# Performance work log

Measured on AMD Instinct MI355X. Metric: run time of the kernel, lower is better.

Reference implementation:

```python
import jax, jax.numpy as jnp
import numpy as np
from jax import lax

B, T, D, LD, K = 128, 1024, 256, 512, 128
RD = LD + K  # 640 residual-LSTM width
PAD = 15     # (31 - 1) // 2 'same' padding for the LSA location conv


def _gru(x, h, wih, whh, bih, bhh):
    # torch.nn.GRUCell semantics, gate order [r, z, n]
    gi = x @ wih.T + bih
    gh = h @ whh.T + bhh
    ir, iz, inn = jnp.split(gi, 3, axis=-1)
    hr, hz, hn = jnp.split(gh, 3, axis=-1)
    r = jax.nn.sigmoid(ir + hr)
    z = jax.nn.sigmoid(iz + hz)
    n = jnp.tanh(inn + r * hn)
    return (1.0 - z) * n + z * h


def _lstm(x, h, c, wih, whh, bih, bhh):
    # torch.nn.LSTMCell semantics, gate order [i, f, g, o]
    g = x @ wih.T + bih + h @ whh.T + bhh
    i, f, gg, o = jnp.split(g, 4, axis=-1)
    c2 = jax.nn.sigmoid(f) * c + jax.nn.sigmoid(i) * jnp.tanh(gg)
    h2 = jax.nn.sigmoid(o) * jnp.tanh(c2)
    return h2, c2


def _forward(encoder_seq, encoder_seq_proj, prenet_in, attn_hidden, rnn1_h, rnn1_c,
             rnn2_h, rnn2_c, res_h, res_c, context_vec, cumulative, attn_prev,
             fc1_w, fc1_b, fc2_w, fc2_b, gru_wih, gru_whh, gru_bih, gru_bhh,
             conv_w, L_w, L_b, W_w, W_b, v_w, ri_w, ri_b,
             r1_wih, r1_whh, r1_bih, r1_bhh, r2_wih, r2_whh, r2_bih, r2_bhh,
             res_wih, res_whh, res_bih, res_bhh, stop_w, stop_b):
    # PreNet (dropout p = 0 in Decoder.__init__, so pure tanh-MLP)
    p = jnp.tanh(prenet_in @ fc1_w.T + fc1_b)
    prenet_out = jnp.tanh(p @ fc2_w.T + fc2_b)                     # [B, D//2]
    # Attention GRU
    attn_in = jnp.concatenate([context_vec, prenet_out], axis=-1)  # [B, D + D//2]
    attn_h = _gru(attn_in, attn_hidden, gru_wih, gru_whh, gru_bih, gru_bhh)  # [B, D]
    # LSA location-sensitive attention (cumulative/attn_prev are zeros at t=0)
    pq = (attn_h @ W_w.T + W_b)[:, None, :]                        # [B, 1, D]
    loc = jnp.stack([cumulative, attn_prev], axis=1)               # [B, 2, T]
    conv_out = lax.conv_general_dilated(loc, conv_w, (1,), [(PAD, PAD)],
                                        dimension_numbers=('NCH', 'OIH', 'NCH'))  # [B, 32, T]
    ploc = jnp.swapaxes(conv_out, 1, 2) @ L_w.T + L_b              # [B, T, D]
    u = jnp.squeeze(jnp.tanh(pq + encoder_seq_proj + ploc) @ v_w.T, -1)  # [B, T]
    sig = jax.nn.sigmoid(u)
    scores = sig / jnp.sum(sig, axis=1, keepdims=True)             # [B, T]
    cum_new = cumulative + scores
    context = jnp.einsum('bt,btd->bd', scores, encoder_seq)        # [B, D]
    # rnn_input projection + two residual LSTM cells (eval: no zoneout)
    x = jnp.concatenate([context, attn_h], axis=1) @ ri_w.T + ri_b  # [B, LD]
    h1, c1 = _lstm(x, rnn1_h, rnn1_c, r1_wih, r1_whh, r1_bih, r1_bhh)
    x = x + h1
    h2, c2 = _lstm(x, rnn2_h, rnn2_c, r2_wih, r2_whh, r2_bih, r2_bhh)
    x = x + h2
    # 4-layer residual LSTM stack on [prenet_in, x]
    res_x = jnp.concatenate([prenet_in, x], axis=1)                # [B, RD]
    hs, cs = [], []
    for i in range(4):
        hi, ci = _lstm(res_x, res_h[i], res_c[i], res_wih[i], res_whh[i], res_bih[i], res_bhh[i])
        res_x = res_x + hi
        hs.append(hi)
        cs.append(ci)
    cond = res_x                                                   # cond_features [B, RD]
    stop = jax.nn.sigmoid(cond @ stop_w.T + stop_b)                # [B, 1]
    return (cond, stop, scores, attn_h, h1, c1, h2, c2,
            jnp.stack(hs), jnp.stack(cs), context, cum_new)


def setup_inputs() -> dict:
    keys = iter(jax.random.split(jax.random.key(0), 64))
    nxt = lambda: next(keys)
    rn = lambda s: jax.random.normal(nxt(), s, jnp.float32)
    wp = lambda s: rn(s) * 0.02
    return {
        'encoder_seq': rn((B, T, D)),
        'encoder_seq_proj': rn((B, T, D)),
        'prenet_in': rn((B, K)),
        'attn_hidden': rn((B, D)),
        'rnn1_h': rn((B, LD)), 'rnn1_c': rn((B, LD)),
        'rnn2_h': rn((B, LD)), 'rnn2_c': rn((B, LD)),
        'res_h': rn((4, B, RD)), 'res_c': rn((4, B, RD)),
        'context_vec': rn((B, D)),
        'cumulative': jnp.zeros((B, T), jnp.float32),
        'attn_prev': jnp.zeros((B, T), jnp.float32),
        'fc1_w': wp((256, K)), 'fc1_b': jnp.zeros((256,), jnp.float32),
        'fc2_w': wp((D // 2, 256)), 'fc2_b': jnp.zeros((D // 2,), jnp.float32),
        'gru_wih': wp((3 * D, D + D // 2)), 'gru_whh': wp((3 * D, D)),
        'gru_bih': jnp.zeros((3 * D,), jnp.float32), 'gru_bhh': jnp.zeros((3 * D,), jnp.float32),
        'conv_w': wp((32, 2, 31)),
        'L_w': wp((D, 32)), 'L_b': jnp.zeros((D,), jnp.float32),
        'W_w': wp((D, D)), 'W_b': jnp.zeros((D,), jnp.float32),
        'v_w': wp((1, D)),
        'ri_w': wp((LD, 2 * D)), 'ri_b': jnp.zeros((LD,), jnp.float32),
        'r1_wih': wp((4 * LD, LD)), 'r1_whh': wp((4 * LD, LD)),
        'r1_bih': jnp.zeros((4 * LD,), jnp.float32), 'r1_bhh': jnp.zeros((4 * LD,), jnp.float32),
        'r2_wih': wp((4 * LD, LD)), 'r2_whh': wp((4 * LD, LD)),
        'r2_bih': jnp.zeros((4 * LD,), jnp.float32), 'r2_bhh': jnp.zeros((4 * LD,), jnp.float32),
        'res_wih': wp((4, 4 * RD, RD)), 'res_whh': wp((4, 4 * RD, RD)),
        'res_bih': jnp.zeros((4, 4 * RD), jnp.float32), 'res_bhh': jnp.zeros((4, 4 * RD), jnp.float32),
        'stop_w': wp((1, RD)), 'stop_b': jnp.zeros((1,), jnp.float32),
    }


def reference(encoder_seq, encoder_seq_proj, prenet_in, attn_hidden, rnn1_h, rnn1_c,
              rnn2_h, rnn2_c, res_h, res_c, context_vec, cumulative, attn_prev,
              fc1_w, fc1_b, fc2_w, fc2_b, gru_wih, gru_whh, gru_bih, gru_bhh,
              conv_w, L_w, L_b, W_w, W_b, v_w, ri_w, ri_b,
              r1_wih, r1_whh, r1_bih, r1_bhh, r2_wih, r2_whh, r2_bih, r2_bhh,
              res_wih, res_whh, res_bih, res_bhh, stop_w, stop_b):
    return _forward(encoder_seq, encoder_seq_proj, prenet_in, attn_hidden, rnn1_h, rnn1_c,
                    rnn2_h, rnn2_c, res_h, res_c, context_vec, cumulative, attn_prev,
                    fc1_w, fc1_b, fc2_w, fc2_b, gru_wih, gru_whh, gru_bih, gru_bhh,
                    conv_w, L_w, L_b, W_w, W_b, v_w, ri_w, ri_b,
                    r1_wih, r1_whh, r1_bih, r1_bhh, r2_wih, r2_whh, r2_bih, r2_bhh,
                    res_wih, res_whh, res_bih, res_bhh, stop_w, stop_b)
```

## Files before the change

### kernel.cpp

```cpp
#include <hip/hip_runtime.h>

#define DEV __device__ __forceinline__

typedef __attribute__((ext_vector_type(8))) short short8;
typedef __attribute__((ext_vector_type(4))) float f32x4;

DEV float fast_rcp(float x) { return __builtin_amdgcn_rcpf(x); }
DEV float sigm(float x) { return fast_rcp(1.0f + __expf(-x)); }
DEV float tanhf_fast(float x) { return 1.0f - 2.0f * fast_rcp(1.0f + __expf(2.0f * x)); }

DEV short f2bf(float f) {
    unsigned u = __float_as_uint(f);
    unsigned r = (u + 0x7FFFu + ((u >> 16) & 1u)) >> 16;
    return (short)r;
}

__global__ __launch_bounds__(256) void gemm2s_kernel(
    const float* __restrict__ A1, int K1, const float* __restrict__ W1, int ldw1,
    const float* __restrict__ A2, int K2, const float* __restrict__ W2, int ldw2,
    float* __restrict__ Cp, int N, int KS, int KC)
{
    __shared__ float As[2][16][128];
    __shared__ float Ws[2][16][33];
    const int tid = threadIdx.x;
    const int chunk = blockIdx.x % KS;
    const int n0 = (blockIdx.x / KS) * 32;
    const int kbeg = chunk * KC;
    const int nt = KC / 16;
    const int tx = tid & 15, ty = tid >> 4;
    const int lm = tid & 127, lk = (tid >> 7) * 8;

    float acc[16];
#pragma unroll
    for (int i = 0; i < 16; ++i) acc[i] = 0.f;

    float4 ra0, ra1, rw;
    auto load_regs = [&](int k0) {
        const float* A; const float* W; int lda, ldw, kc;
        if (k0 < K1) { A = A1; W = W1; lda = K1; ldw = ldw1; kc = k0; }
        else         { A = A2; W = W2; lda = K2; ldw = ldw2; kc = k0 - K1; }
        ra0 = *(const float4*)(A + (size_t)lm * lda + kc + lk);
        ra1 = *(const float4*)(A + (size_t)lm * lda + kc + lk + 4);
        if (tid < 128) {
            int nl = tid >> 2, kq = (tid & 3) * 4;
            rw = *(const float4*)(W + (size_t)(n0 + nl) * ldw + kc + kq);
        }
    };
    auto store_lds = [&](int buf) {
        As[buf][lk + 0][lm] = ra0.x; As[buf][lk + 1][lm] = ra0.y;
        As[buf][lk + 2][lm] = ra0.z; As[buf][lk + 3][lm] = ra0.w;
        As[buf][lk + 4][lm] = ra1.x; As[buf][lk + 5][lm] = ra1.y;
        As[buf][lk + 6][lm] = ra1.z; As[buf][lk + 7][lm] = ra1.w;
        if (tid < 128) {
            int nl = tid >> 2, kq = (tid & 3) * 4;
            Ws[buf][kq + 0][nl] = rw.x; Ws[buf][kq + 1][nl] = rw.y;
            Ws[buf][kq + 2][nl] = rw.z; Ws[buf][kq + 3][nl] = rw.w;
        }
    };

    load_regs(kbeg);
    store_lds(0);
    __syncthreads();

    for (int it = 0; it < nt; ++it) {
        const int cur = it & 1;
        if (it + 1 < nt) load_regs(kbeg + (it + 1) * 16);
#pragma unroll
        for (int kk = 0; kk < 16; ++kk) {
            float w0 = Ws[cur][kk][tx * 2 + 0];
            float w1 = Ws[cur][kk][tx * 2 + 1];
            float4 x0 = *(const float4*)&As[cur][kk][ty * 8];
            float4 x1 = *(const float4*)&As[cur][kk][ty * 8 + 4];
            acc[0] += x0.x * w0; acc[1] += x0.y * w0;
            acc[2] += x0.z * w0; acc[3] += x0.w * w0;
            acc[4] += x1.x * w0; acc[5] += x1.y * w0;
            acc[6] += x1.z * w0; acc[7] += x1.w * w0;
            acc[8]  += x0.x * w1; acc[9]  += x0.y * w1;
            acc[10] += x0.z * w1; acc[11] += x0.w * w1;
            acc[12] += x1.x * w1; acc[13] += x1.y * w1;
            acc[14] += x1.z * w1; acc[15] += x1.w * w1;
        }
        if (it + 1 < nt) store_lds(cur ^ 1);
        __syncthreads();
    }

    float* Co = Cp + (size_t)chunk * 128 * N;
#pragma unroll
    for (int j = 0; j < 2; ++j) {
        int n = n0 + tx * 2 + j;
#pragma unroll
        for (int i = 0; i < 8; ++i)
            Co[(size_t)(ty * 8 + i) * N + n] = acc[j * 8 + i];
    }
}

__global__ void reduce_act_kernel(const float* __restrict__ p, int KS, int MN,
                                  const float* __restrict__ b,
                                  float* __restrict__ out, int N, int act)
{
    int idx = blockIdx.x * 256 + threadIdx.x;
    if (idx >= MN) return;
    int n = idx % N;
    float v = b ? b[n] : 0.f;
    for (int s = 0; s < KS; ++s) v += p[(size_t)s * MN + idx];
    if (act) v = tanhf_fast(v);
    out[idx] = v;
}

__global__ void gru_gate_kernel(const float* __restrict__ gi_p, int KSi,
                                const float* __restrict__ gh_p, int KSh,
                                const float* __restrict__ bih, const float* __restrict__ bhh,
                                const float* __restrict__ h, float* __restrict__ out)
{
    const size_t MN = 128 * 768;
    int m = blockIdx.x, d = threadIdx.x;
    size_t base = (size_t)m * 768 + d;
    float ir = bih[d], iz = bih[256 + d], in = bih[512 + d];
    for (int s = 0; s < KSi; ++s) {
        const float* p = gi_p + s * MN + base;
        ir += p[0]; iz += p[256]; in += p[512];
    }
    float hr = bhh[d], hz = bhh[256 + d], hn = bhh[512 + d];
    for (int s = 0; s < KSh; ++s) {
        const float* p = gh_p + s * MN + base;
        hr += p[0]; hz += p[256]; hn += p[512];
    }
    float r = sigm(ir + hr);
    float z = sigm(iz + hz);
    float n = tanhf_fast(in + r * hn);
    out[m * 256 + d] = (1.f - z) * n + z * h[m * 256 + d];
}

__global__ void lstm_gate_kernel(const float* __restrict__ gp, int KS,
                                 const float* __restrict__ bih, const float* __restrict__ bhh,
                                 const float* __restrict__ c_in,
                                 float* __restrict__ h_out, float* __restrict__ c_out,
                                 float* __restrict__ xacc, int H)
{
    int d = blockIdx.x * 256 + threadIdx.x;
    int m = blockIdx.y;
    if (d >= H) return;
    const size_t MN = (size_t)128 * 4 * H;
    size_t base = (size_t)m * 4 * H + d;
    float iv = bih[d] + bhh[d];
    float fv = bih[H + d] + bhh[H + d];
    float gv = bih[2 * H + d] + bhh[2 * H + d];
    float ov = bih[3 * H + d] + bhh[3 * H + d];
    for (int s = 0; s < KS; ++s) {
        const float* p = gp + s * MN + base;
        iv += p[0]; fv += p[H]; gv += p[2 * H]; ov += p[3 * H];
    }
    float c2 = sigm(fv) * c_in[m * H + d] + sigm(iv) * tanhf_fast(gv);
    float h2 = sigm(ov) * tanhf_fast(c2);
    h_out[m * H + d] = h2;
    c_out[m * H + d] = c2;
    if (xacc) xacc[m * H + d] += h2;
}

__global__ void lw_bf16_kernel(const float* __restrict__ Lw, short* __restrict__ LwBf)
{
    int i = blockIdx.x * 256 + threadIdx.x;
    LwBf[i] = f2bf(Lw[i]);
}

__global__ __launch_bounds__(256) void attn_u_kernel(
    const float* __restrict__ esp, const float* __restrict__ pq,
    const short* __restrict__ LwBf, const float* __restrict__ Lb,
    const float* __restrict__ vw, const float* __restrict__ cw,
    const float* __restrict__ cum, const float* __restrict__ prev,
    float* __restrict__ sig_out)
{
    const int b = blockIdx.x >> 4;
    const int t0 = (blockIdx.x & 15) << 6;
    const int tid = threadIdx.x;

    __shared__ float cum_s[94], prev_s[94];
    __shared__ float cw_s[2][32][33];
    __shared__ short conv_bf[64 * 32];
    __shared__ short lw_bf[256 * 32];
    __shared__ float pq_s[256], vw_s[256];

    if (tid < 94) {
        int ti = t0 - 15 + tid;
        cum_s[tid] = (ti >= 0 && ti < 1024) ? cum[b * 1024 + ti] : 0.f;
    } else if (tid >= 128 && tid < 222) {
        int i = tid - 128;
        int ti = t0 - 15 + i;
        prev_s[i] = (ti >= 0 && ti < 1024) ? prev[b * 1024 + ti] : 0.f;
    }
    for (int i = tid; i < 2048; i += 256) {
        int which = i >> 10, c = (i >> 5) & 31, k = i & 31;
        cw_s[which][c][k] = (k < 31) ? cw[(c * 2 + which) * 31 + k] : 0.f;
    }
    {
        const int4* src = (const int4*)LwBf;
        int4* dst = (int4*)lw_bf;
#pragma unroll
        for (int k = 0; k < 4; ++k) dst[tid + k * 256] = src[tid + k * 256];
    }
    pq_s[tid] = pq[b * 256 + tid] + Lb[tid];
    vw_s[tid] = vw[tid];
    __syncthreads();

    {
        int c = tid & 31, t8 = (tid >> 5) << 3;
        float a[8] = {0.f, 0.f, 0.f, 0.f, 0.f, 0.f, 0.f, 0.f};
        for (int k = 0; k < 31; ++k) {
            float w0 = cw_s[0][c][k], w1 = cw_s[1][c][k];
#pragma unroll
            for (int j = 0; j < 8; ++j)
                a[j] += w0 * cum_s[t8 + j + k] + w1 * prev_s[t8 + j + k];
        }
#pragma unroll
        for (int j = 0; j < 8; ++j) conv_bf[(t8 + j) * 32 + c] = f2bf(a[j]);
    }
    __syncthreads();

    const int lane = tid & 63, w = tid >> 6;
    const int q = lane >> 4, c16 = lane & 15;
    const int myt = t0 + w * 16 + c16;

    short8 bfrag = *(const short8*)&conv_bf[(w * 16 + c16) * 32 + q * 8];
    const float* er = esp + ((size_t)(b * 1024 + myt) << 8);

    float s = 0.f;
#pragma unroll
    for (int dt = 0; dt < 16; ++dt) {
        short8 afrag = *(const short8*)&lw_bf[(dt * 16 + c16) * 32 + q * 8];
        f32x4 acc = {0.f, 0.f, 0.f, 0.f};
        acc = __builtin_amdgcn_mfma_f32_16x16x32_bf16(afrag, bfrag, acc, 0, 0, 0);
        const int d0 = dt * 16 + q * 4;
        float4 e   = *(const float4*)(er + d0);
        float4 pqv = *(const float4*)&pq_s[d0];
        float4 vwv = *(const float4*)&vw_s[d0];
        s += tanhf_fast(pqv.x + e.x + acc[0]) * vwv.x;
        s += tanhf_fast(pqv.y + e.y + acc[1]) * vwv.y;
        s += tanhf_fast(pqv.z + e.z + acc[2]) * vwv.z;
        s += tanhf_fast(pqv.w + e.w + acc[3]) * vwv.w;
    }
    s += __shfl_xor(s, 16);
    s += __shfl_xor(s, 32);
    if (lane < 16)
        sig_out[b * 1024 + t0 + w * 16 + lane] = sigm(s);
}

__global__ void attn_norm_kernel(const float* __restrict__ sig, const float* __restrict__ cum,
                                 float* __restrict__ scores, float* __restrict__ cum_new,
                                 float* __restrict__ ctx)
{
    __shared__ float red[4];
    int b = blockIdx.x, tid = threadIdx.x;
    float4 sv = *(const float4*)&sig[b * 1024 + tid * 4];
    float s = sv.x + sv.y + sv.z + sv.w;
#pragma unroll
    for (int off = 1; off < 64; off <<= 1) s += __shfl_xor(s, off);
    if ((tid & 63) == 0) red[tid >> 6] = s;
    __syncthreads();
    float inv = fast_rcp(red[0] + red[1] + red[2] + red[3]);
    float4 cv = *(const float4*)&cum[b * 1024 + tid * 4];
    float4 sc = {sv.x * inv, sv.y * inv, sv.z * inv, sv.w * inv};
    *(float4*)&scores[b * 1024 + tid * 4] = sc;
    float4 cn = {cv.x + sc.x, cv.y + sc.y, cv.z + sc.z, cv.w + sc.w};
    *(float4*)&cum_new[b * 1024 + tid * 4] = cn;
    ctx[b * 256 + tid] = 0.f;
}

__global__ void attn_ctx_kernel(const float* __restrict__ scores, const float* __restrict__ es,
                                float* __restrict__ ctx)
{
    __shared__ float sc_s[128];
    int b = blockIdx.x >> 3;
    int tbase = (blockIdx.x & 7) * 128;
    int tid = threadIdx.x;
    if (tid < 128) sc_s[tid] = scores[b * 1024 + tbase + tid];
    __syncthreads();
    float a = 0.f;
    const float* ep = es + ((size_t)(b * 1024 + tbase)) * 256 + tid;
#pragma unroll 4
    for (int tt = 0; tt < 128; ++tt)
        a += sc_s[tt] * ep[(size_t)tt * 256];
    atomicAdd(&ctx[b * 256 + tid], a);
}

__global__ void build_rescat_kernel(const float* __restrict__ pre, const float* __restrict__ x,
                                    float* __restrict__ res)
{
    int idx = blockIdx.x * 256 + threadIdx.x;
    int m = idx / 640, d = idx - m * 640;
    res[idx] = (d < 128) ? pre[m * 128 + d] : x[m * 512 + d - 128];
}

__global__ void copy_kernel(const float* __restrict__ src, float* __restrict__ dst, int n)
{
    int idx = blockIdx.x * 256 + threadIdx.x;
    if (idx < n) dst[idx] = src[idx];
}

__global__ void stop_kernel(const float* __restrict__ res, const float* __restrict__ sw,
                            const float* __restrict__ sb, float* __restrict__ stop)
{
    int m = blockIdx.x, lane = threadIdx.x;
    float s = 0.f;
    for (int k = lane; k < 640; k += 64) s += res[m * 640 + k] * sw[k];
#pragma unroll
    for (int off = 1; off < 64; off <<= 1) s += __shfl_xor(s, off);
    if (lane == 0) stop[m] = sigm(s + sb[0]);
}

extern "C" void kernel_launch(void* const* d_in, const int* in_sizes, int n_in,
                              void* d_out, int out_size, void* d_ws, size_t ws_size,
                              hipStream_t stream)
{
    const float* encoder_seq      = (const float*)d_in[0];
    const float* encoder_seq_proj = (const float*)d_in[1];
    const float* prenet_in        = (const float*)d_in[2];
    const float* attn_hidden      = (const float*)d_in[3];
    const float* rnn1_h  = (const float*)d_in[4];
    const float* rnn1_c  = (const float*)d_in[5];
    const float* rnn2_h  = (const float*)d_in[6];
    const float* rnn2_c  = (const float*)d_in[7];
    const float* res_h   = (const float*)d_in[8];
    const float* res_c   = (const float*)d_in[9];
    const float* context_vec = (const float*)d_in[10];
    const float* cumulative  = (const float*)d_in[11];
    const float* attn_prev   = (const float*)d_in[12];
    const float* fc1_w = (const float*)d_in[13];
    const float* fc1_b = (const float*)d_in[14];
    const float* fc2_w = (const float*)d_in[15];
    const float* fc2_b = (const float*)d_in[16];
    const float* gru_wih = (const float*)d_in[17];
    const float* gru_whh = (const float*)d_in[18];
    const float* gru_bih = (const float*)d_in[19];
    const float* gru_bhh = (const float*)d_in[20];
    const float* conv_w = (const float*)d_in[21];
    const float* L_w = (const float*)d_in[22];
    const float* L_b = (const float*)d_in[23];
    const float* W_w = (const float*)d_in[24];
    const float* W_b = (const float*)d_in[25];
    const float* v_w = (const float*)d_in[26];
    const float* ri_w = (const float*)d_in[27];
    const float* ri_b = (const float*)d_in[28];
    const float* r1_wih = (const float*)d_in[29];
    const float* r1_whh = (const float*)d_in[30];
    const float* r1_bih = (const float*)d_in[31];
    const float* r1_bhh = (const float*)d_in[32];
    const float* r2_wih = (const float*)d_in[33];
    const float* r2_whh = (const float*)d_in[34];
    const float* r2_bih = (const float*)d_in[35];
    const float* r2_bhh = (const float*)d_in[36];
    const float* res_wih = (const float*)d_in[37];
    const float* res_whh = (const float*)d_in[38];
    const float* res_bih = (const float*)d_in[39];
    const float* res_bhh = (const float*)d_in[40];
    const float* stop_w = (const float*)d_in[41];
    const float* stop_b = (const float*)d_in[42];

    float* ws  = (float*)d_ws;
    float* out = (float*)d_out;

    const size_t OFF_P    = 0;
    const size_t OFF_POUT = 32768;
    const size_t OFF_PQ   = 49152;
    const size_t OFF_SIG  = 81920;
    const size_t OFF_X    = 212992;
    const size_t OFF_RES  = 278528;
    const size_t OFF_LWT  = 360448;
    const size_t OFF_PART = 368640;
    const size_t OFF_PARTB = OFF_PART + (size_t)8 * 128 * 768;

    const size_t O_COND   = 0;
    const size_t O_STOP   = 81920;
    const size_t O_SCORES = 82048;
    const size_t O_ATTNH  = 213120;
    const size_t O_H1     = 245888;
    const size_t O_C1     = 311424;
    const size_t O_H2     = 376960;
    const size_t O_C2     = 442496;
    const size_t O_HS     = 508032;
    const size_t O_CS     = 835712;
    const size_t O_CTX    = 1163392;
    const size_t O_CUM    = 1196160;

    short* lwbf = (short*)(ws + OFF_LWT);
    lw_bf16_kernel<<<32, 256, 0, stream>>>(L_w, lwbf);

    gemm2s_kernel<<<8 * 4, 256, 0, stream>>>(prenet_in, 128, fc1_w, 128,
                                             nullptr, 0, nullptr, 0,
                                             ws + OFF_PART, 256, 4, 32);
    reduce_act_kernel<<<128, 256, 0, stream>>>(ws + OFF_PART, 4, 128 * 256, fc1_b,
                                               ws + OFF_P, 256, 1);
    gemm2s_kernel<<<4 * 8, 256, 0, stream>>>(ws + OFF_P, 256, fc2_w, 256,
                                             nullptr, 0, nullptr, 0,
                                             ws + OFF_PART, 128, 8, 32);
    reduce_act_kernel<<<64, 256, 0, stream>>>(ws + OFF_PART, 8, 128 * 128, fc2_b,
                                              ws + OFF_POUT, 128, 1);

    gemm2s_kernel<<<24 * 8, 256, 0, stream>>>(context_vec, 256, gru_wih, 384,
                                              ws + OFF_POUT, 128, gru_wih + 256, 384,
                                              ws + OFF_PART, 768, 8, 48);
    gemm2s_kernel<<<24 * 8, 256, 0, stream>>>(attn_hidden, 256, gru_whh, 256,
                                              nullptr, 0, nullptr, 0,
                                              ws + OFF_PARTB, 768, 8, 32);
    gru_gate_kernel<<<128, 256, 0, stream>>>(ws + OFF_PART, 8, ws + OFF_PARTB, 8,
                                             gru_bih, gru_bhh, attn_hidden, out + O_ATTNH);

    gemm2s_kernel<<<8 * 8, 256, 0, stream>>>(out + O_ATTNH, 256, W_w, 256,
                                             nullptr, 0, nullptr, 0,
                                             ws + OFF_PART, 256, 8, 32);
    reduce_act_kernel<<<128, 256, 0, stream>>>(ws + OFF_PART, 8, 128 * 256, W_b,
                                               ws + OFF_PQ, 256, 0);

    attn_u_kernel<<<2048, 256, 0, stream>>>(encoder_seq_proj, ws + OFF_PQ, lwbf,
                                            L_b, v_w, conv_w, cumulative, attn_prev,
                                            ws + OFF_SIG);
    attn_norm_kernel<<<128, 256, 0, stream>>>(ws + OFF_SIG, cumulative,
                                              out + O_SCORES, out + O_CUM, out + O_CTX);
    attn_ctx_kernel<<<1024, 256, 0, stream>>>(out + O_SCORES, encoder_seq, out + O_CTX);

    gemm2s_kernel<<<16 * 8, 256, 0, stream>>>(out + O_CTX, 256, ri_w, 512,
                                              out + O_ATTNH, 256, ri_w + 256, 512,
                                              ws + OFF_PART, 512, 8, 64);
    reduce_act_kernel<<<256, 256, 0, stream>>>(ws + OFF_PART, 8, 128 * 512, ri_b,
                                               ws + OFF_X, 512, 0);

    gemm2s_kernel<<<64 * 8, 256, 0, stream>>>(ws + OFF_X, 512, r1_wih, 512,
                                              rnn1_h, 512, r1_whh, 512,
                                              ws + OFF_PART, 2048, 8, 128);
    lstm_gate_kernel<<<dim3(2, 128), 256, 0, stream>>>(ws + OFF_PART, 8, r1_bih, r1_bhh,
                                                       rnn1_c, out + O_H1, out + O_C1,
                                                       ws + OFF_X, 512);
    gemm2s_kernel<<<64 * 8, 256, 0, stream>>>(ws + OFF_X, 512, r2_wih, 512,
                                              rnn2_h, 512, r2_whh, 512,
                                              ws + OFF_PART, 2048, 8, 128);
    lstm_gate_kernel<<<dim3(2, 128), 256, 0, stream>>>(ws + OFF_PART, 8, r2_bih, r2_bhh,
                                                       rnn2_c, out + O_H2, out + O_C2,
                                                       ws + OFF_X, 512);

    build_rescat_kernel<<<320, 256, 0, stream>>>(prenet_in, ws + OFF_X, ws + OFF_RES);

    for (int i = 0; i < 4; ++i) {
        const float* wih = res_wih + (size_t)i * 2560 * 640;
        const float* whh = res_whh + (size_t)i * 2560 * 640;
        gemm2s_kernel<<<80 * 8, 256, 0, stream>>>(ws + OFF_RES, 640, wih, 640,
                                                  res_h + (size_t)i * 81920, 640, whh, 640,
                                                  ws + OFF_PART, 2560, 8, 160);
        lstm_gate_kernel<<<dim3(3, 128), 256, 0, stream>>>(ws + OFF_PART, 8,
                                                           res_bih + (size_t)i * 2560,
                                                           res_bhh + (size_t)i * 2560,
                                                           res_c + (size_t)i * 81920,
                                                           out + O_HS + (size_t)i * 81920,
                                                           out + O_CS + (size_t)i * 81920,
                                                           ws + OFF_RES, 640);
    }

    copy_kernel<<<320, 256, 0, stream>>>(ws + OFF_RES, out + O_COND, 128 * 640);
    stop_kernel<<<128, 64, 0, stream>>>(ws + OFF_RES, stop_w, stop_b, out + O_STOP);
}
```

Before: 662.4 us.

## Replace FP32 SIMT GEMMs with split-bf16 MFMA GEMMs and fuse residual plumbing

Replaces the LDS-tiled FP32 FMA GEMM with an MFMA-based core that splits each fp32 operand into bf16 hi/lo parts and issues three bf16 MFMAs to approximate fp32 accuracy. The two GRU GEMMs are merged into one launch. The L_w bf16 conversion moves inside the attention kernel. The LSTM gate kernel now writes the residual sum into fresh ping-pong buffers, which removes the rescat build, in-place update and final copy kernels. Split-K factors also change, and the residual LSTM GEMMs are split into separate ih and hh launches. The 3-term bf16 split loses a little precision compared with pure fp32, and each attention block now redundantly converts L_w.

```diff
diff --git a/kernel.cpp b/kernel.cpp
--- a/kernel.cpp
+++ b/kernel.cpp
@@ -14,84 +14,121 @@
     unsigned r = (u + 0x7FFFu + ((u >> 16) & 1u)) >> 16;
     return (short)r;
 }
-
-__global__ __launch_bounds__(256) void gemm2s_kernel(
+DEV float bf2f(short h) {
+    return __uint_as_float(((unsigned)(unsigned short)h) << 16);
+}
+DEV void split1(float f, short& h, short& l) {
+    h = f2bf(f);
+    l = f2bf(f - bf2f(h));
+}
+DEV void split8(const float4& x0, const float4& x1, short8& h, short8& l) {
+    float fv[8] = {x0.x, x0.y, x0.z, x0.w, x1.x, x1.y, x1.z, x1.w};
+#pragma unroll
+    for (int j = 0; j < 8; ++j) { short hh, ll; split1(fv[j], hh, ll); h[j] = hh; l[j] = ll; }
+}
+#define MFMA16 __builtin_amdgcn_mfma_f32_16x16x32_bf16
+DEV f32x4 mfma3(const short8& ah, const short8& al, const short8& bh, const short8& bl, f32x4 acc) {
+    acc = MFMA16(ah, bh, acc, 0, 0, 0);
+    acc = MFMA16(al, bh, acc, 0, 0, 0);
+    acc = MFMA16(ah, bl, acc, 0, 0, 0);
+    return acc;
+}
+
+DEV void gemm_core(int bx,
+                   const float* __restrict__ A1, int K1,
+                   const float* __restrict__ W1, int ldw1,
+                   const float* __restrict__ A2, int K2,
+                   const float* __restrict__ W2, int ldw2,
+                   float* __restrict__ Cp, int N, int KS, int KC)
+{
+    const int tid = threadIdx.x;
+    const int chunk = bx % KS;
+    const int n0 = (bx / KS) * 32;
+    const int kbeg = chunk * KC;
+    const int w = tid >> 6, lane = tid & 63;
+    const int q = lane >> 4, r = lane & 15;
+    const int m_base = w * 32;
+
+    f32x4 acc[2][2];
+#pragma unroll
+    for (int mt = 0; mt < 2; ++mt)
+#pragma unroll
+        for (int nt = 0; nt < 2; ++nt)
+            acc[mt][nt] = (f32x4){0.f, 0.f, 0.f, 0.f};
+
+    auto load_frag = [&](int kg, float4 (&a)[2][2], float4 (&wv)[2][2]) {
+        const float* A; const float* W; int lda, ldw, kc;
+        if (kg < K1) { A = A1; W = W1; lda = K1; ldw = ldw1; kc = kg; }
+        else         { A = A2; W = W2; lda = K2; ldw = ldw2; kc = kg - K1; }
+#pragma unroll
+        for (int mt = 0; mt < 2; ++mt) {
+            const float* ap = A + (size_t)(m_base + mt * 16 + r) * lda + kc + q * 8;
+            a[mt][0] = *(const float4*)ap;
+            a[mt][1] = *(const float4*)(ap + 4);
+        }
+#pragma unroll
+        for (int nt = 0; nt < 2; ++nt) {
+            const float* wp = W + (size_t)(n0 + nt * 16 + r) * ldw + kc + q * 8;
+            wv[nt][0] = *(const float4*)wp;
+            wv[nt][1] = *(const float4*)(wp + 4);
+        }
+    };
+
+    auto compute = [&](const float4 (&a)[2][2], const float4 (&wv)[2][2]) {
+        short8 bh[2], bl[2];
+#pragma unroll
+        for (int nt = 0; nt < 2; ++nt) split8(wv[nt][0], wv[nt][1], bh[nt], bl[nt]);
+#pragma unroll
+        for (int mt = 0; mt < 2; ++mt) {
+            short8 ah, al;
+            split8(a[mt][0], a[mt][1], ah, al);
+#pragma unroll
+            for (int nt = 0; nt < 2; ++nt)
+                acc[mt][nt] = mfma3(ah, al, bh[nt], bl[nt], acc[mt][nt]);
+        }
+    };
+
+    float4 aA[2][2], aB[2][2], wA[2][2], wB[2][2];
+    const int nsteps = KC >> 5;
+
+    load_frag(kbeg, aA, wA);
+    for (int s = 0; s + 1 < nsteps; ++s) {
+        if (s & 1) { load_frag(kbeg + (s + 1) * 32, aA, wA); compute(aB, wB); }
+        else       { load_frag(kbeg + (s + 1) * 32, aB, wB); compute(aA, wA); }
+    }
+    if ((nsteps - 1) & 1) compute(aB, wB);
+    else                  compute(aA, wA);
+
+    float* Co = Cp + (size_t)chunk * 128 * N;
+#pragma unroll
+    for (int mt = 0; mt < 2; ++mt)
+#pragma unroll
+        for (int nt = 0; nt < 2; ++nt)
+#pragma unroll
+            for (int i = 0; i < 4; ++i)
+                Co[(size_t)(m_base + mt * 16 + q * 4 + i) * N + n0 + nt * 16 + r] = acc[mt][nt][i];
+}
+
+__global__ __launch_bounds__(256) void gemm_one_kernel(
     const float* __restrict__ A1, int K1, const float* __restrict__ W1, int ldw1,
     const float* __restrict__ A2, int K2, const float* __restrict__ W2, int ldw2,
     float* __restrict__ Cp, int N, int KS, int KC)
 {
-    __shared__ float As[2][16][128];
-    __shared__ float Ws[2][16][33];
-    const int tid = threadIdx.x;
-    const int chunk = blockIdx.x % KS;
-    const int n0 = (blockIdx.x / KS) * 32;
-    const int kbeg = chunk * KC;
-    const int nt = KC / 16;
-    const int tx = tid & 15, ty = tid >> 4;
-    const int lm = tid & 127, lk = (tid >> 7) * 8;
-
-    float acc[16];
-#pragma unroll
-    for (int i = 0; i < 16; ++i) acc[i] = 0.f;
-
-    float4 ra0, ra1, rw;
-    auto load_regs = [&](int k0) {
-        const float* A; const float* W; int lda, ldw, kc;
-        if (k0 < K1) { A = A1; W = W1; lda = K1; ldw = ldw1; kc = k0; }
-        else         { A = A2; W = W2; lda = K2; ldw = ldw2; kc = k0 - K1; }
-        ra0 = *(const float4*)(A + (size_t)lm * lda + kc + lk);
-        ra1 = *(const float4*)(A + (size_t)lm * lda + kc + lk + 4);
-        if (tid < 128) {
-            int nl = tid >> 2, kq = (tid & 3) * 4;
-            rw = *(const float4*)(W + (size_t)(n0 + nl) * ldw + kc + kq);
-        }
-    };
-    auto store_lds = [&](int buf) {
-        As[buf][lk + 0][lm] = ra0.x; As[buf][lk + 1][lm] = ra0.y;
-        As[buf][lk + 2][lm] = ra0.z; As[buf][lk + 3][lm] = ra0.w;
-        As[buf][lk + 4][lm] = ra1.x; As[buf][lk + 5][lm] = ra1.y;
-        As[buf][lk + 6][lm] = ra1.z; As[buf][lk + 7][lm] = ra1.w;
-        if (tid < 128) {
-            int nl = tid >> 2, kq = (tid & 3) * 4;
-            Ws[buf][kq + 0][nl] = rw.x; Ws[buf][kq + 1][nl] = rw.y;
-            Ws[buf][kq + 2][nl] = rw.z; Ws[buf][kq + 3][nl] = rw.w;
-        }
-    };
-
-    load_regs(kbeg);
-    store_lds(0);
-    __syncthreads();
-
-    for (int it = 0; it < nt; ++it) {
-        const int cur = it & 1;
-        if (it + 1 < nt) load_regs(kbeg + (it + 1) * 16);
-#pragma unroll
-        for (int kk = 0; kk < 16; ++kk) {
-            float w0 = Ws[cur][kk][tx * 2 + 0];
-            float w1 = Ws[cur][kk][tx * 2 + 1];
-            float4 x0 = *(const float4*)&As[cur][kk][ty * 8];
-            float4 x1 = *(const float4*)&As[cur][kk][ty * 8 + 4];
-            acc[0] += x0.x * w0; acc[1] += x0.y * w0;
-            acc[2] += x0.z * w0; acc[3] += x0.w * w0;
-            acc[4] += x1.x * w0; acc[5] += x1.y * w0;
-            acc[6] += x1.z * w0; acc[7] += x1.w * w0;
-            acc[8]  += x0.x * w1; acc[9]  += x0.y * w1;
-            acc[10] += x0.z * w1; acc[11] += x0.w * w1;
-            acc[12] += x1.x * w1; acc[13] += x1.y * w1;
-            acc[14] += x1.z * w1; acc[15] += x1.w * w1;
-        }
-        if (it + 1 < nt) store_lds(cur ^ 1);
-        __syncthreads();
-    }
-
-    float* Co = Cp + (size_t)chunk * 128 * N;
-#pragma unroll
-    for (int j = 0; j < 2; ++j) {
-        int n = n0 + tx * 2 + j;
-#pragma unroll
-        for (int i = 0; i < 8; ++i)
-            Co[(size_t)(ty * 8 + i) * N + n] = acc[j * 8 + i];
-    }
+    gemm_core(blockIdx.x, A1, K1, W1, ldw1, A2, K2, W2, ldw2, Cp, N, KS, KC);
+}
+
+__global__ __launch_bounds__(256) void gemm_gru_kernel(
+    const float* __restrict__ ctx, const float* __restrict__ pout,
+    const float* __restrict__ h_old,
+    const float* __restrict__ wih, const float* __restrict__ whh,
+    float* __restrict__ Pa, float* __restrict__ Pb)
+{
+    if (blockIdx.x < 288)
+        gemm_core(blockIdx.x, ctx, 256, wih, 384, pout, 128, wih + 256, 384,
+                  Pa, 768, 12, 32);
+    else
+        gemm_core(blockIdx.x - 288, h_old, 256, whh, 256, nullptr, 0, nullptr, 0,
+                  Pb, 768, 8, 32);
 }
 
 __global__ void reduce_act_kernel(const float* __restrict__ p, int KS, int MN,
@@ -135,7 +172,9 @@
                                  const float* __restrict__ bih, const float* __restrict__ bhh,
                                  const float* __restrict__ c_in,
                                  float* __restrict__ h_out, float* __restrict__ c_out,
-                                 float* __restrict__ xacc, int H)
+                                 const float* __restrict__ xa, int sa,
+                                 const float* __restrict__ xb, int sb, int split,
+                                 float* __restrict__ x_new, int H)
 {
     int d = blockIdx.x * 256 + threadIdx.x;
     int m = blockIdx.y;
@@ -150,22 +189,17 @@
         const float* p = gp + s * MN + base;
         iv += p[0]; fv += p[H]; gv += p[2 * H]; ov += p[3 * H];
     }
-    float c2 = sigm(fv) * c_in[m * H + d] + sigm(iv) * tanhf_fast(gv);
+    float c2 = sigm(fv) * c_in[(size_t)m * H + d] + sigm(iv) * tanhf_fast(gv);
     float h2 = sigm(ov) * tanhf_fast(c2);
-    h_out[m * H + d] = h2;
-    c_out[m * H + d] = c2;
-    if (xacc) xacc[m * H + d] += h2;
-}
-
-__global__ void lw_bf16_kernel(const float* __restrict__ Lw, short* __restrict__ LwBf)
-{
-    int i = blockIdx.x * 256 + threadIdx.x;
-    LwBf[i] = f2bf(Lw[i]);
+    h_out[(size_t)m * H + d] = h2;
+    c_out[(size_t)m * H + d] = c2;
+    float xo = (d < split) ? xa[(size_t)m * sa + d] : xb[(size_t)m * sb + d - split];
+    x_new[(size_t)m * H + d] = xo + h2;
 }
 
 __global__ __launch_bounds__(256) void attn_u_kernel(
     const float* __restrict__ esp, const float* __restrict__ pq,
-    const short* __restrict__ LwBf, const float* __restrict__ Lb,
+    const float* __restrict__ Lw, const float* __restrict__ Lb,
     const float* __restrict__ vw, const float* __restrict__ cw,
     const float* __restrict__ cum, const float* __restrict__ prev,
     float* __restrict__ sig_out)
@@ -193,10 +227,16 @@
         cw_s[which][c][k] = (k < 31) ? cw[(c * 2 + which) * 31 + k] : 0.f;
     }
     {
-        const int4* src = (const int4*)LwBf;
-        int4* dst = (int4*)lw_bf;
-#pragma unroll
-        for (int k = 0; k < 4; ++k) dst[tid + k * 256] = src[tid + k * 256];
+        const float4* src = (const float4*)Lw;
+#pragma unroll
+        for (int k = 0; k < 8; ++k) {
+            float4 v = src[tid + k * 256];
+            int base = (tid + k * 256) * 4;
+            lw_bf[base + 0] = f2bf(v.x);
+            lw_bf[base + 1] = f2bf(v.y);
+            lw_bf[base + 2] = f2bf(v.z);
+            lw_bf[base + 3] = f2bf(v.w);
+        }
     }
     pq_s[tid] = pq[b * 256 + tid] + Lb[tid];
     vw_s[tid] = vw[tid];
@@ -228,7 +268,7 @@
     for (int dt = 0; dt < 16; ++dt) {
         short8 afrag = *(const short8*)&lw_bf[(dt * 16 + c16) * 32 + q * 8];
         f32x4 acc = {0.f, 0.f, 0.f, 0.f};
-        acc = __builtin_amdgcn_mfma_f32_16x16x32_bf16(afrag, bfrag, acc, 0, 0, 0);
+        acc = MFMA16(afrag, bfrag, acc, 0, 0, 0);
         const int d0 = dt * 16 + q * 4;
         float4 e   = *(const float4*)(er + d0);
         float4 pqv = *(const float4*)&pq_s[d0];
@@ -280,20 +320,6 @@
     for (int tt = 0; tt < 128; ++tt)
         a += sc_s[tt] * ep[(size_t)tt * 256];
     atomicAdd(&ctx[b * 256 + tid], a);
-}
-
-__global__ void build_rescat_kernel(const float* __restrict__ pre, const float* __restrict__ x,
-                                    float* __restrict__ res)
-{
-    int idx = blockIdx.x * 256 + threadIdx.x;
-    int m = idx / 640, d = idx - m * 640;
-    res[idx] = (d < 128) ? pre[m * 128 + d] : x[m * 512 + d - 128];
-}
-
-__global__ void copy_kernel(const float* __restrict__ src, float* __restrict__ dst, int n)
-{
-    int idx = blockIdx.x * 256 + threadIdx.x;
-    if (idx < n) dst[idx] = src[idx];
 }
 
 __global__ void stop_kernel(const float* __restrict__ res, const float* __restrict__ sw,
@@ -358,15 +384,18 @@
     float* ws  = (float*)d_ws;
     float* out = (float*)d_out;
 
-    const size_t OFF_P    = 0;
-    const size_t OFF_POUT = 32768;
-    const size_t OFF_PQ   = 49152;
-    const size_t OFF_SIG  = 81920;
-    const size_t OFF_X    = 212992;
-    const size_t OFF_RES  = 278528;
-    const size_t OFF_LWT  = 360448;
-    const size_t OFF_PART = 368640;
-    const size_t OFF_PARTB = OFF_PART + (size_t)8 * 128 * 768;
+    const size_t OFF_P     = 0;
+    const size_t OFF_POUT  = 32768;
+    const size_t OFF_PQ    = 49152;
+    const size_t OFF_SIG   = 81920;
+    const size_t OFF_X     = 212992;
+    const size_t OFF_XB    = 278528;
+    const size_t OFF_XC    = 344064;
+    const size_t OFF_R0    = 409600;
+    const size_t OFF_R1    = 491520;
+    const size_t OFF_PART  = 573440;
+    const size_t OFF_PARTB = OFF_PART + (size_t)12 * 128 * 768;
+    const size_t OFF_PARTH = OFF_PART + (size_t)4 * 128 * 2560;
 
     const size_t O_COND   = 0;
     const size_t O_STOP   = 81920;
@@ -381,78 +410,88 @@
     const size_t O_CTX    = 1163392;
     const size_t O_CUM    = 1196160;
 
-    short* lwbf = (short*)(ws + OFF_LWT);
-    lw_bf16_kernel<<<32, 256, 0, stream>>>(L_w, lwbf);
-
-    gemm2s_kernel<<<8 * 4, 256, 0, stream>>>(prenet_in, 128, fc1_w, 128,
-                                             nullptr, 0, nullptr, 0,
-                                             ws + OFF_PART, 256, 4, 32);
+    gemm_one_kernel<<<8 * 4, 256, 0, stream>>>(
+        prenet_in, 128, fc1_w, 128, nullptr, 0, nullptr, 0,
+        ws + OFF_PART, 256, 4, 32);
     reduce_act_kernel<<<128, 256, 0, stream>>>(ws + OFF_PART, 4, 128 * 256, fc1_b,
                                                ws + OFF_P, 256, 1);
-    gemm2s_kernel<<<4 * 8, 256, 0, stream>>>(ws + OFF_P, 256, fc2_w, 256,
-                                             nullptr, 0, nullptr, 0,
-                                             ws + OFF_PART, 128, 8, 32);
+    gemm_one_kernel<<<4 * 8, 256, 0, stream>>>(
+        ws + OFF_P, 256, fc2_w, 256, nullptr, 0, nullptr, 0,
+        ws + OFF_PART, 128, 8, 32);
     reduce_act_kernel<<<64, 256, 0, stream>>>(ws + OFF_PART, 8, 128 * 128, fc2_b,
                                               ws + OFF_POUT, 128, 1);
 
-    gemm2s_kernel<<<24 * 8, 256, 0, stream>>>(context_vec, 256, gru_wih, 384,
-                                              ws + OFF_POUT, 128, gru_wih + 256, 384,
-                                              ws + OFF_PART, 768, 8, 48);
-    gemm2s_kernel<<<24 * 8, 256, 0, stream>>>(attn_hidden, 256, gru_whh, 256,
-                                              nullptr, 0, nullptr, 0,
-                                              ws + OFF_PARTB, 768, 8, 32);
-    gru_gate_kernel<<<128, 256, 0, stream>>>(ws + OFF_PART, 8, ws + OFF_PARTB, 8,
+    gemm_gru_kernel<<<480, 256, 0, stream>>>(
+        context_vec, ws + OFF_POUT, attn_hidden, gru_wih, gru_whh,
+        ws + OFF_PART, ws + OFF_PARTB);
+    gru_gate_kernel<<<128, 256, 0, stream>>>(ws + OFF_PART, 12, ws + OFF_PARTB, 8,
                                              gru_bih, gru_bhh, attn_hidden, out + O_ATTNH);
 
-    gemm2s_kernel<<<8 * 8, 256, 0, stream>>>(out + O_ATTNH, 256, W_w, 256,
-                                             nullptr, 0, nullptr, 0,
-                                             ws + OFF_PART, 256, 8, 32);
+    gemm_one_kernel<<<8 * 8, 256, 0, stream>>>(
+        out + O_ATTNH, 256, W_w, 256, nullptr, 0, nullptr, 0,
+        ws + OFF_PART, 256, 8, 32);
     reduce_act_kernel<<<128, 256, 0, stream>>>(ws + OFF_PART, 8, 128 * 256, W_b,
                                                ws + OFF_PQ, 256, 0);
 
-    attn_u_kernel<<<2048, 256, 0, stream>>>(encoder_seq_proj, ws + OFF_PQ, lwbf,
+    attn_u_kernel<<<2048, 256, 0, stream>>>(encoder_seq_proj, ws + OFF_PQ, L_w,
                                             L_b, v_w, conv_w, cumulative, attn_prev,
                                             ws + OFF_SIG);
     attn_norm_kernel<<<128, 256, 0, stream>>>(ws + OFF_SIG, cumulative,
                                               out + O_SCORES, out + O_CUM, out + O_CTX);
     attn_ctx_kernel<<<1024, 256, 0, stream>>>(out + O_SCORES, encoder_seq, out + O_CTX);
 
-    gemm2s_kernel<<<16 * 8, 256, 0, stream>>>(out + O_CTX, 256, ri_w, 512,
-                                              out + O_ATTNH, 256, ri_w + 256, 512,
-                                              ws + OFF_PART, 512, 8, 64);
+    gemm_one_kernel<<<16 * 8, 256, 0, stream>>>(
+        out + O_CTX, 256, ri_w, 512,
+        out + O_ATTNH, 256, ri_w + 256, 512,
+        ws + OFF_PART, 512, 8, 64);
     reduce_act_kernel<<<256, 256, 0, stream>>>(ws + OFF_PART, 8, 128 * 512, ri_b,
                                                ws + OFF_X, 512, 0);
 
-    gemm2s_kernel<<<64 * 8, 256, 0, stream>>>(ws + OFF_X, 512, r1_wih, 512,
-                                              rnn1_h, 512, r1_whh, 512,
-                                              ws + OFF_PART, 2048, 8, 128);
-    lstm_gate_kernel<<<dim3(2, 128), 256, 0, stream>>>(ws + OFF_PART, 8, r1_bih, r1_bhh,
-                                                       rnn1_c, out + O_H1, out + O_C1,
-                                                       ws + OFF_X, 512);
-    gemm2s_kernel<<<64 * 8, 256, 0, stream>>>(ws + OFF_X, 512, r2_wih, 512,
-                                              rnn2_h, 512, r2_whh, 512,
-                                              ws + OFF_PART, 2048, 8, 128);
-    lstm_gate_kernel<<<dim3(2, 128), 256, 0, stream>>>(ws + OFF_PART, 8, r2_bih, r2_bhh,
-                                                       rnn2_c, out + O_H2, out + O_C2,
-                                                       ws + OFF_X, 512);
-
-    build_rescat_kernel<<<320, 256, 0, stream>>>(prenet_in, ws + OFF_X, ws + OFF_RES);
+    gemm_one_kernel<<<64 * 4, 256, 0, stream>>>(
+        ws + OFF_X, 512, r1_wih, 512,
+        rnn1_h, 512, r1_whh, 512,
+        ws + OFF_PART, 2048, 4, 256);
+    lstm_gate_kernel<<<dim3(2, 128), 256, 0, stream>>>(
+        ws + OFF_PART, 4, r1_bih, r1_bhh, rnn1_c, out + O_H1, out + O_C1,
+        nullptr, 0, ws + OFF_X, 512, 0, ws + OFF_XB, 512);
+    gemm_one_kernel<<<64 * 4, 256, 0, stream>>>(
+        ws + OFF_XB, 512, r2_wih, 512,
+        rnn2_h, 512, r2_whh, 512,
+        ws + OFF_PART, 2048, 4, 256);
+    lstm_gate_kernel<<<dim3(2, 128), 256, 0, stream>>>(
+        ws + OFF_PART, 4, r2_bih, r2_bhh, rnn2_c, out + O_H2, out + O_C2,
+        nullptr, 0, ws + OFF_XB, 512, 0, ws + OFF_XC, 512);
 
     for (int i = 0; i < 4; ++i) {
         const float* wih = res_wih + (size_t)i * 2560 * 640;
         const float* whh = res_whh + (size_t)i * 2560 * 640;
-        gemm2s_kernel<<<80 * 8, 256, 0, stream>>>(ws + OFF_RES, 640, wih, 640,
-                                                  res_h + (size_t)i * 81920, 640, whh, 640,
-                                                  ws + OFF_PART, 2560, 8, 160);
-        lstm_gate_kernel<<<dim3(3, 128), 256, 0, stream>>>(ws + OFF_PART, 8,
-                                                           res_bih + (size_t)i * 2560,
-                                                           res_bhh + (size_t)i * 2560,
-                                                           res_c + (size_t)i * 81920,
-                                                           out + O_HS + (size_t)i * 81920,
-                                                           out + O_CS + (size_t)i * 81920,
-                                                           ws + OFF_RES, 640);
-    }
-
-    copy_kernel<<<320, 256, 0, stream>>>(ws + OFF_RES, out + O_COND, 128 * 640);
-    stop_kernel<<<128, 64, 0, stream>>>(ws + OFF_RES, stop_w, stop_b, out + O_STOP);
-}
+        const float* hA  = res_h + (size_t)i * 81920;
+        const float* cA  = res_c + (size_t)i * 81920;
+        if (i == 0) {
+            gemm_one_kernel<<<80 * 4, 256, 0, stream>>>(
+                prenet_in, 128, wih, 640,
+                ws + OFF_XC, 512, wih + 128, 640,
+                ws + OFF_PART, 2560, 4, 160);
+        } else {
+            const float* rcur = ws + ((i & 1) ? OFF_R0 : OFF_R1);
+            gemm_one_kernel<<<80 * 4, 256, 0, stream>>>(
+                rcur, 640, wih, 640, nullptr, 0, nullptr, 0,
+                ws + OFF_PART, 2560, 4, 160);
+        }
+        gemm_one_kernel<<<80 * 4, 256, 0, stream>>>(
+            hA, 640, whh, 640, nullptr, 0, nullptr, 0,
+            ws + OFF_PARTH, 2560, 4, 160);
+
+        const float *xa, *xb; int sa, sb, split;
+        if (i == 0) { xa = prenet_in; sa = 128; xb = ws + OFF_XC; sb = 512; split = 128; }
+        else { xa = nullptr; sa = 0; xb = ws + ((i & 1) ? OFF_R0 : OFF_R1); sb = 640; split = 0; }
+        float* xnew = (i == 3) ? (out + O_COND) : (ws + ((i & 1) ? OFF_R1 : OFF_R0));
+        lstm_gate_kernel<<<dim3(3, 128), 256, 0, stream>>>(
+            ws + OFF_PART, 8,
+            res_bih + (size_t)i * 2560, res_bhh + (size_t)i * 2560,
+            cA, out + O_HS + (size_t)i * 81920, out + O_CS + (size_t)i * 81920,
+            xa, sa, xb, sb, split, xnew, 640);
+    }
+
+    stop_kernel<<<128, 64, 0, stream>>>(out + O_COND, stop_w, stop_b, out + O_STOP);
+}
```

Result: faster. 632.8 us (-4.5%).
